# Optimization experiments

Hardware: AMD Instinct MI355X
Metric: run time of the kernel (lower is better)

Reference implementation:

```python
import jax, jax.numpy as jnp
import numpy as np

# PEPS grid configuration (matches init_kwargs)
X, Y = 4, 4            # xnodes, ynodes
D = 6                  # bond_dim
P = 2                  # features_in (physical dim)
F = 10                 # features_out (forced by result.view([10]))
CX, CY = X // 2, Y // 2  # center node carries the output leg
BATCH = 2048


def node_labels(i, j):
    # bond labels after the physical index is contracted away; axis order: up, left, down, right, out
    labs = []
    if i > 0: labs.append(f'v{i-1}_{j}')   # up bond (shared with row i-1)
    if j > 0: labs.append(f'h{i}_{j-1}')   # left bond (shared with col j-1)
    if i < X - 1: labs.append(f'v{i}_{j}') # down bond
    if j < Y - 1: labs.append(f'h{i}_{j}') # right bond
    if (i, j) == (CX, CY): labs.append('o')  # output leg on center node
    return labs


def node_shape(i, j):
    shp = [P]  # physical axis first (input_nodes[i][j][0] ^ peps_nodes[i][j][0])
    shp += [D] * (int(i > 0) + int(j > 0) + int(i < X - 1) + int(j < Y - 1))
    if (i, j) == (CX, CY): shp.append(F)
    return tuple(shp)


def setup_inputs() -> dict:
    key = jax.random.key(0)
    keys = jax.random.split(key, X * Y + 1)
    inp = {"x": jax.random.normal(keys[0], (BATCH, X, Y, P), dtype=jnp.float32)}
    k = 1
    for i in range(X):
        for j in range(Y):
            # simple_peps uniform init with std=0.01
            inp[f"w{i}{j}"] = jax.random.uniform(keys[k], node_shape(i, j), dtype=jnp.float32, minval=-0.01, maxval=0.01)
            k += 1
    return inp


def _td(a, alabs, b, blabs):
    """Label-tracked tensordot over all shared bond labels."""
    shared = [l for l in alabs if l in blabs]
    ai = [alabs.index(l) for l in shared]
    bi = [blabs.index(l) for l in shared]
    out = jnp.tensordot(a, b, axes=(ai, bi))
    labs = [l for l in alabs if l not in shared] + [l for l in blabs if l not in shared]
    return out, labs


def _contract_sample(xs, ws):
    # xs: [X, Y, P] one sample; ws: list-of-lists of node tensors
    # 1) contract each input vector into its PEPS node over the physical axis,
    #    then L2-normalize each contracted node (as in func())
    nodes = []
    for i in range(X):
        row = []
        for j in range(Y):
            t = jnp.tensordot(xs[i, j], ws[i][j], axes=(0, 0))
            t = t / jnp.linalg.norm(t)
            row.append(t)
        nodes.append(row)
    # 2) exact contraction of the 2D network, row-by-row boundary sweep
    cur, labs = nodes[0][0], node_labels(0, 0)
    for j in range(1, Y):
        cur, labs = _td(cur, labs, nodes[0][j], node_labels(0, j))
    for i in range(1, X):
        for j in range(Y):
            cur, labs = _td(cur, labs, nodes[i][j], node_labels(i, j))
    out = cur.reshape(F)  # result.view([10])
    return out / jnp.linalg.norm(out)


def reference(x, w00, w01, w02, w03, w10, w11, w12, w13,
              w20, w21, w22, w23, w30, w31, w32, w33):
    ws = [[w00, w01, w02, w03],
          [w10, w11, w12, w13],
          [w20, w21, w22, w23],
          [w30, w31, w32, w33]]
    return jax.vmap(lambda s: _contract_sample(s, ws))(x)  # [B, F]
```

## Files before the change

kernel.cpp:

```cpp
#include <hip/hip_runtime.h>
#include <math.h>

#define NTHREADS 256

struct PW {
    const float* w[16];
    int perp[16];
};

__global__ __launch_bounds__(NTHREADS) void gram64(PW pw, float* __restrict__ g) {
    const int n = blockIdx.x >> 2, sl = blockIdx.x & 3;
    const float* __restrict__ W = pw.w[n];
    const int m = pw.perp[n];
    float s00 = 0.f, s01 = 0.f, s11 = 0.f;
    for (int e = (sl * NTHREADS + threadIdx.x) * 4; e < m; e += NTHREADS * 16) {
        const float4 a = *reinterpret_cast<const float4*>(W + e);
        const float4 b = *reinterpret_cast<const float4*>(W + m + e);
        s00 += a.x * a.x + a.y * a.y + a.z * a.z + a.w * a.w;
        s01 += a.x * b.x + a.y * b.y + a.z * b.z + a.w * b.w;
        s11 += b.x * b.x + b.y * b.y + b.z * b.z + b.w * b.w;
    }
    for (int off = 32; off > 0; off >>= 1) {
        s00 += __shfl_down(s00, off, 64);
        s01 += __shfl_down(s01, off, 64);
        s11 += __shfl_down(s11, off, 64);
    }
    __shared__ float red[4][3];
    const int lane = threadIdx.x & 63, wv = threadIdx.x >> 6;
    if (lane == 0) { red[wv][0] = s00; red[wv][1] = s01; red[wv][2] = s11; }
    __syncthreads();
    if (threadIdx.x == 0) {
        float t0 = 0.f, t1 = 0.f, t2 = 0.f;
        for (int i = 0; i < 4; i++) { t0 += red[i][0]; t1 += red[i][1]; t2 += red[i][2]; }
        g[n * 12 + sl * 3 + 0] = t0; g[n * 12 + sl * 3 + 1] = t1; g[n * 12 + sl * 3 + 2] = t2;
    }
}

constexpr int SA = 0, SB = 1296, SC = 2592;
constexpr int SP = 3888, SQ = 4104, SX = 4320, SY = 4536, SZ = 4752;
constexpr int ARENA = 4968;

template<int TOT, int DST>
__device__ __forceinline__ void stg_id(float* __restrict__ lds, const float* __restrict__ W,
                                       float a0, float b0, float a1, float b1, int tid) {
    constexpr int QUADS = TOT / 4;
    for (int e = tid; e < 2 * QUADS; e += NTHREADS) {
        const int s = (e >= QUADS);
        const int p = e - s * QUADS;
        const float al = s ? a1 : a0, be = s ? b1 : b0;
        const float4 u0 = *reinterpret_cast<const float4*>(W + 4 * p);
        const float4 u1 = *reinterpret_cast<const float4*>(W + TOT + 4 * p);
        float4 rv;
        rv.x = al * u0.x + be * u1.x; rv.y = al * u0.y + be * u1.y;
        rv.z = al * u0.z + be * u1.z; rv.w = al * u0.w + be * u1.w;
        *reinterpret_cast<float4*>(lds + s * ARENA + DST + 4 * p) = rv;
    }
}

template<int D0, int D1, int D2, int D3, int S0, int S1, int S2, int S3, int DST>
__device__ __forceinline__ void stg_pm(float* __restrict__ lds, const float* __restrict__ W,
                                       float a0, float b0, float a1, float b1, int tid) {
    constexpr int TOT = D0 * D1 * D2 * D3;
    for (int e = tid; e < 2 * TOT; e += NTHREADS) {
        const int s = (e >= TOT);
        const int d = e - s * TOT;
        int r = d;
        const int i3 = r % D3; r /= D3;
        const int i2 = r % D2; r /= D2;
        const int i1 = r % D1;
        const int i0 = r / D1;
        const int src = i0 * S0 + i1 * S1 + i2 * S2 + i3 * S3;
        const float al = s ? a1 : a0, be = s ? b1 : b0;
        lds[s * ARENA + DST + d] = al * W[src] + be * W[TOT + src];
    }
}

template<int M, int N, int K, int TM, int TN, int AOFF, int BOFF>
__device__ __forceinline__ void mm_acc(const float* __restrict__ lds, int tid,
                                       float (&acc)[TM][TN]) {
    constexpr int WM = M / TM, WN = N / TN, PER_S = WM * WN, TOT = 2 * PER_S;
    static_assert(TOT <= NTHREADS, "tile overflow");
    static_assert(M % TM == 0 && N % TN == 0, "tile divide");
    if (tid >= TOT) return;
    const int s = (tid >= PER_S);
    const int r = tid - s * PER_S;
    const int mt = r / WN, nt = r - mt * WN;
    const float* __restrict__ Ab = lds + s * ARENA + AOFF + mt * TM;
    const float* __restrict__ Bb = lds + s * ARENA + BOFF + nt * TN;
#pragma unroll
    for (int i = 0; i < TM; i++)
#pragma unroll
        for (int j = 0; j < TN; j++) acc[i][j] = 0.f;
#pragma unroll 6
    for (int k = 0; k < K; ++k) {
        float a[TM], b[TN];
        if constexpr (TM == 4) {
            const float4 v = *reinterpret_cast<const float4*>(Ab + k * M);
            a[0] = v.x; a[1] = v.y; a[2] = v.z; a[3] = v.w;
        } else {
            const float2 v = *reinterpret_cast<const float2*>(Ab + k * M);
            a[0] = v.x; a[1] = v.y;
        }
        if constexpr (TN == 4) {
            const float4 v = *reinterpret_cast<const float4*>(Bb + k * N);
            b[0] = v.x; b[1] = v.y; b[2] = v.z; b[3] = v.w;
        } else {
            const float2 v = *reinterpret_cast<const float2*>(Bb + k * N);
            b[0] = v.x; b[1] = v.y;
        }
#pragma unroll
        for (int i = 0; i < TM; i++)
#pragma unroll
            for (int j = 0; j < TN; j++) acc[i][j] += a[i] * b[j];
    }
}

template<int M, int N, int TM, int TN,
         int NM2, int OSM1, int OSM2, int NN2, int OSN1, int OSN2, int OOFF>
__device__ __forceinline__ void mm_wr(float* __restrict__ lds, int tid,
                                      const float (&acc)[TM][TN]) {
    constexpr int WM = M / TM, WN = N / TN, PER_S = WM * WN, TOT = 2 * PER_S;
    if (tid >= TOT) return;
    const int s = (tid >= PER_S);
    const int r = tid - s * PER_S;
    const int mt = r / WN, nt = r - mt * WN;
    float* __restrict__ Ob = lds + s * ARENA + OOFF;
    constexpr bool NCONT = (TN == 4) && (OSN2 == 1) && ((NN2 >= N) || (OSN1 == NN2));
    constexpr bool MCONT = (TM == 4) && (OSM2 == 1) && ((NM2 >= M) || (OSM1 == NM2));
    if constexpr (NCONT) {
        const int nb = nt * TN;
#pragma unroll
        for (int i = 0; i < TM; i++) {
            const int m = mt * TM + i;
            int m1, m2;
            if constexpr (NM2 >= M) { m1 = 0; m2 = m; }
            else                    { m1 = m / NM2; m2 = m - m1 * NM2; }
            float4 v; v.x = acc[i][0]; v.y = acc[i][1]; v.z = acc[i][2]; v.w = acc[i][3];
            *reinterpret_cast<float4*>(Ob + m1 * OSM1 + m2 * OSM2 + nb) = v;
        }
    } else if constexpr (MCONT) {
        const int mb = mt * TM;
#pragma unroll
        for (int j = 0; j < TN; j++) {
            const int n = nt * TN + j;
            int n1, n2;
            if constexpr (NN2 >= N) { n1 = 0; n2 = n; }
            else                    { n1 = n / NN2; n2 = n - n1 * NN2; }
            float4 v; v.x = acc[0][j]; v.y = acc[1][j]; v.z = acc[2][j]; v.w = acc[3][j];
            *reinterpret_cast<float4*>(Ob + n1 * OSN1 + n2 * OSN2 + mb) = v;
        }
    } else {
#pragma unroll
        for (int i = 0; i < TM; i++) {
            const int m = mt * TM + i;
            int m1, m2;
            if constexpr (NM2 >= M) { m1 = 0; m2 = m; }
            else                    { m1 = m / NM2; m2 = m - m1 * NM2; }
#pragma unroll
            for (int j = 0; j < TN; j++) {
                const int n = nt * TN + j;
                int n1, n2;
                if constexpr (NN2 >= N) { n1 = 0; n2 = n; }
                else                    { n1 = n / NN2; n2 = n - n1 * NN2; }
                Ob[m1 * OSM1 + m2 * OSM2 + n1 * OSN1 + n2 * OSN2] = acc[i][j];
            }
        }
    }
}

template<int M, int N, int K, int TM, int TN,
         int NM2, int OSM1, int OSM2, int NN2, int OSN1, int OSN2,
         int AOFF, int BOFF, int OOFF>
__device__ __forceinline__ void mmd(float* __restrict__ lds, int tid) {
    float acc[TM][TN];
    mm_acc<M, N, K, TM, TN, AOFF, BOFF>(lds, tid, acc);
    mm_wr<M, N, TM, TN, NM2, OSM1, OSM2, NN2, OSN1, OSN2, OOFF>(lds, tid, acc);
}

__global__ __launch_bounds__(NTHREADS, 4) void peps_main(const float* __restrict__ x, PW pw,
                                                         const float* __restrict__ gram,
                                                         float* __restrict__ out) {
    __shared__ float lds[2 * ARENA];
    __shared__ float cfa[2][16], cfb[2][16];
    __shared__ float red[4][2][10];

    const int tid = threadIdx.x;
    const int s0 = blockIdx.x * 2;

    if (tid < 32) {
        const int sl = tid >> 4, n = tid & 15;
        const float a = x[(s0 + sl) * 32 + n * 2 + 0];
        const float b = x[(s0 + sl) * 32 + n * 2 + 1];
        float g0 = 0.f, g1 = 0.f, g2 = 0.f;
#pragma unroll
        for (int q = 0; q < 4; q++) {
            g0 += gram[n * 12 + q * 3 + 0];
            g1 += gram[n * 12 + q * 3 + 1];
            g2 += gram[n * 12 + q * 3 + 2];
        }
        const float inv = 1.f / sqrtf(a * a * g0 + 2.f * a * b * g1 + b * b * g2);
        cfa[sl][n] = a * inv; cfb[sl][n] = b * inv;
    }
    __syncthreads();

#define CF(WI) cfa[0][WI], cfb[0][WI], cfa[1][WI], cfb[1][WI]

    stg_pm<1, 1, 6, 6, 0, 0, 1, 6, SQ + 0>(lds, pw.w[0], CF(0), tid);
    stg_id<216, SX>(lds, pw.w[1], CF(1), tid);
    stg_id<216, SY>(lds, pw.w[4], CF(4), tid);
    stg_id<1296, SA>(lds, pw.w[5], CF(5), tid);
    __syncthreads();

    mmd<6, 36, 6, 2, 4, 6, 0, 36, 36, 0, 1, SQ + 0, SX, SP>(lds, tid);
    stg_pm<1, 6, 6, 6, 0, 1, 36, 6, SZ>(lds, pw.w[2], CF(2), tid);
    stg_id<36, SQ + 36>(lds, pw.w[3], CF(3), tid);
    __syncthreads();

    mmd<36, 36, 6, 4, 4, 6, 216, 6, 6, 1, 36, SP, SY, SB>(lds, tid);
    stg_id<216, SX>(lds, pw.w[7], CF(7), tid);
    stg_pm<6, 6, 6, 6, 216, 1, 36, 6, SC>(lds, pw.w[6], CF(6), tid);
    stg_id<36, SQ + 72>(lds, pw.w[12], CF(12), tid);
    __syncthreads();

    {
        float a3[4][4];
        mm_acc<36, 36, 36, 4, 4, SB, SA>(lds, tid, a3);
        mmd<36, 6, 6, 4, 2, 36, 0, 1, 6, 0, 36, SZ, SQ + 36, SP>(lds, tid);
        stg_pm<1, 6, 6, 6, 0, 6, 36, 1, SY>(lds, pw.w[8], CF(8), tid);
        __syncthreads();
        mm_wr<36, 36, 4, 4, 6, 216, 6, 6, 1, 36, SA>(lds, tid, a3);
    }
    __syncthreads();

    mmd<36, 36, 6, 4, 4, 6, 6, 216, 6, 36, 1, SP, SX, SB>(lds, tid);
    stg_pm<1, 6, 6, 6, 0, 6, 36, 1, SZ>(lds, pw.w[13], CF(13), tid);
    __syncthreads();

    {
        float a6[4][4];
        mm_acc<36, 36, 36, 4, 4, SC, SB>(lds, tid, a6);
        mmd<6, 36, 6, 2, 4, 6, 0, 36, 36, 0, 1, SQ + 72, SY, SP>(lds, tid);
        stg_id<36, SQ + 108>(lds, pw.w[15], CF(15), tid);
        stg_pm<1, 6, 6, 6, 0, 1, 36, 6, SX>(lds, pw.w[11], CF(11), tid);
        __syncthreads();
        mm_wr<36, 36, 4, 4, 6, 36, 6, 6, 216, 1, SB>(lds, tid, a6);
    }
    __syncthreads();

    {
        float a7[4][4];
        mm_acc<36, 36, 36, 4, 4, SA, SB>(lds, tid, a7);
        stg_pm<6, 6, 6, 6, 36, 6, 216, 1, SC>(lds, pw.w[9], CF(9), tid);
        stg_pm<1, 6, 6, 6, 0, 1, 36, 6, SY>(lds, pw.w[14], CF(14), tid);
        __syncthreads();
        mm_wr<36, 36, 4, 4, 6, 216, 36, 6, 6, 1, SA>(lds, tid, a7);
    }
    __syncthreads();

    {
        float a12[4][2];
        mm_acc<36, 6, 6, 4, 2, SX, SQ + 108>(lds, tid, a12);
        mmd<36, 36, 6, 4, 4, 6, 6, 216, 6, 36, 1, SP, SZ, SB>(lds, tid);
        __syncthreads();
        mm_wr<36, 6, 4, 2, 36, 0, 1, 6, 0, 36, SQ>(lds, tid, a12);
    }
    __syncthreads();

    {
        float a10[4][4], a13[4][4];
        mm_acc<36, 36, 36, 4, 4, SB, SC>(lds, tid, a10);
        mm_acc<36, 36, 6, 4, 4, SQ, SY>(lds, tid, a13);
        __syncthreads();
        mm_wr<36, 36, 4, 4, 6, 216, 6, 6, 36, 1, SC>(lds, tid, a10);
        mm_wr<36, 36, 4, 4, 6, 216, 1, 6, 6, 36, SB>(lds, tid, a13);
    }
    __syncthreads();

    {
        float a11[4][4];
        mm_acc<36, 36, 36, 4, 4, SA, SC>(lds, tid, a11);
        __syncthreads();
        mm_wr<36, 36, 4, 4, 6, 6, 216, 6, 36, 1, SA>(lds, tid, a11);
    }
    __syncthreads();

    {
        float a14[4][4];
        mm_acc<36, 36, 36, 4, 4, SA, SB>(lds, tid, a14);
        __syncthreads();
        mm_wr<36, 36, 4, 4, 6, 216, 36, 6, 6, 1, SA>(lds, tid, a14);
    }
    __syncthreads();

    {
        const float a0 = cfa[0][10], b0 = cfb[0][10];
        const float a1 = cfa[1][10], b1 = cfb[1][10];
        const float* __restrict__ w0 = pw.w[10];
        const float* __restrict__ w1 = w0 + 12960;
        float p0[10], p1[10];
#pragma unroll
        for (int o = 0; o < 10; o++) { p0[o] = 0.f; p1[o] = 0.f; }
        for (int f = tid; f < 324; f += NTHREADS) {
            const float4 E0 = *reinterpret_cast<const float4*>(lds + SA + 4 * f);
            const float4 E1 = *reinterpret_cast<const float4*>(lds + ARENA + SA + 4 * f);
            const float e0[4] = {E0.x, E0.y, E0.z, E0.w};
            const float e1[4] = {E1.x, E1.y, E1.z, E1.w};
#pragma unroll
            for (int u = 0; u < 4; u++) {
                const int e = 4 * f + u;
                const float* __restrict__ q0 = w0 + e * 10;
                const float* __restrict__ q1 = w1 + e * 10;
#pragma unroll
                for (int o = 0; o < 10; o++) {
                    const float v0 = q0[o], v1 = q1[o];
                    p0[o] += e0[u] * (a0 * v0 + b0 * v1);
                    p1[o] += e1[u] * (a1 * v0 + b1 * v1);
                }
            }
        }
#pragma unroll
        for (int o = 0; o < 10; o++)
            for (int off = 32; off > 0; off >>= 1) {
                p0[o] += __shfl_down(p0[o], off, 64);
                p1[o] += __shfl_down(p1[o], off, 64);
            }
        const int lane = tid & 63, wv = tid >> 6;
        if (lane == 0) {
#pragma unroll
            for (int o = 0; o < 10; o++) { red[wv][0][o] = p0[o]; red[wv][1][o] = p1[o]; }
        }
        __syncthreads();
        if (tid < 2) {
            float r[10];
            float ss = 0.f;
#pragma unroll
            for (int o = 0; o < 10; o++) {
                r[o] = red[0][tid][o] + red[1][tid][o] + red[2][tid][o] + red[3][tid][o];
                ss += r[o] * r[o];
            }
            const float inv = 1.f / sqrtf(ss);
#pragma unroll
            for (int o = 0; o < 10; o++) out[(s0 + tid) * 10 + o] = r[o] * inv;
        }
    }
#undef CF
}

extern "C" void kernel_launch(void* const* d_in, const int* in_sizes, int n_in,
                              void* d_out, int out_size, void* d_ws, size_t ws_size,
                              hipStream_t stream) {
    PW pw;
    for (int k = 0; k < 16; k++) {
        pw.w[k] = (const float*)d_in[1 + k];
        pw.perp[k] = in_sizes[1 + k] / 2;
    }
    float* gram = (float*)d_ws;
    gram64<<<64, NTHREADS, 0, stream>>>(pw, gram);

    const float* x = (const float*)d_in[0];
    const int B = out_size / 10;
    peps_main<<<B / 2, NTHREADS, 0, stream>>>(x, pw, gram, (float*)d_out);
}
```

Measured before the change: 134.3 us.

## Read weight operands directly from global in matmuls and reorder contraction schedule

Adds matmul variants that fold the physical-index contraction (alpha*W0 + beta*W1) into the operand load straight from global memory, so identity-layout node tensors are no longer staged into LDS first. The contraction order is also reorganised to match: the LDS arena is re-laid out, stg_id is removed, and the number of barrier-separated phases changes. The aim is to cut LDS staging traffic and some barriers. In exchange, every thread tile now re-reads weights from global/L2 inside the inner loop, which may cost more than the staging it replaces.

```diff
diff --git a/kernel.cpp b/kernel.cpp
--- a/kernel.cpp
+++ b/kernel.cpp
@@ -36,26 +36,9 @@
     }
 }
 
-constexpr int SA = 0, SB = 1296, SC = 2592;
-constexpr int SP = 3888, SQ = 4104, SX = 4320, SY = 4536, SZ = 4752;
-constexpr int ARENA = 4968;
-
-template<int TOT, int DST>
-__device__ __forceinline__ void stg_id(float* __restrict__ lds, const float* __restrict__ W,
-                                       float a0, float b0, float a1, float b1, int tid) {
-    constexpr int QUADS = TOT / 4;
-    for (int e = tid; e < 2 * QUADS; e += NTHREADS) {
-        const int s = (e >= QUADS);
-        const int p = e - s * QUADS;
-        const float al = s ? a1 : a0, be = s ? b1 : b0;
-        const float4 u0 = *reinterpret_cast<const float4*>(W + 4 * p);
-        const float4 u1 = *reinterpret_cast<const float4*>(W + TOT + 4 * p);
-        float4 rv;
-        rv.x = al * u0.x + be * u1.x; rv.y = al * u0.y + be * u1.y;
-        rv.z = al * u0.z + be * u1.z; rv.w = al * u0.w + be * u1.w;
-        *reinterpret_cast<float4*>(lds + s * ARENA + DST + 4 * p) = rv;
-    }
-}
+constexpr int SA = 0, SB = 1296, SC = 2592, SP = 3888;
+constexpr int W0A = 4104, W2A = 4140, W20A = 4356, W31A = 4572, W3A = 4788;
+constexpr int ARENA = 5004;
 
 template<int D0, int D1, int D2, int D3, int S0, int S1, int S2, int S3, int DST>
 __device__ __forceinline__ void stg_pm(float* __restrict__ lds, const float* __restrict__ W,
@@ -80,7 +63,6 @@
                                        float (&acc)[TM][TN]) {
     constexpr int WM = M / TM, WN = N / TN, PER_S = WM * WN, TOT = 2 * PER_S;
     static_assert(TOT <= NTHREADS, "tile overflow");
-    static_assert(M % TM == 0 && N % TN == 0, "tile divide");
     if (tid >= TOT) return;
     const int s = (tid >= PER_S);
     const int r = tid - s * PER_S;
@@ -100,6 +82,96 @@
         } else {
             const float2 v = *reinterpret_cast<const float2*>(Ab + k * M);
             a[0] = v.x; a[1] = v.y;
+        }
+        if constexpr (TN == 4) {
+            const float4 v = *reinterpret_cast<const float4*>(Bb + k * N);
+            b[0] = v.x; b[1] = v.y; b[2] = v.z; b[3] = v.w;
+        } else {
+            const float2 v = *reinterpret_cast<const float2*>(Bb + k * N);
+            b[0] = v.x; b[1] = v.y;
+        }
+#pragma unroll
+        for (int i = 0; i < TM; i++)
+#pragma unroll
+            for (int j = 0; j < TN; j++) acc[i][j] += a[i] * b[j];
+    }
+}
+
+template<int M, int N, int K, int TM, int TN, int AOFF, int PL>
+__device__ __forceinline__ void mm_accGB(const float* __restrict__ lds,
+                                         const float* __restrict__ W,
+                                         float a0, float b0, float a1, float b1,
+                                         int tid, float (&acc)[TM][TN]) {
+    constexpr int WM = M / TM, WN = N / TN, PER_S = WM * WN, TOT = 2 * PER_S;
+    static_assert(TOT <= NTHREADS, "tile overflow");
+    if (tid >= TOT) return;
+    const int s = (tid >= PER_S);
+    const int r = tid - s * PER_S;
+    const int mt = r / WN, nt = r - mt * WN;
+    const float al = s ? a1 : a0, be = s ? b1 : b0;
+    const float* __restrict__ Ab = lds + s * ARENA + AOFF + mt * TM;
+    const float* __restrict__ Bb = W + nt * TN;
+#pragma unroll
+    for (int i = 0; i < TM; i++)
+#pragma unroll
+        for (int j = 0; j < TN; j++) acc[i][j] = 0.f;
+#pragma unroll 6
+    for (int k = 0; k < K; ++k) {
+        float a[TM], b[TN];
+        if constexpr (TM == 4) {
+            const float4 v = *reinterpret_cast<const float4*>(Ab + k * M);
+            a[0] = v.x; a[1] = v.y; a[2] = v.z; a[3] = v.w;
+        } else {
+            const float2 v = *reinterpret_cast<const float2*>(Ab + k * M);
+            a[0] = v.x; a[1] = v.y;
+        }
+        if constexpr (TN == 4) {
+            const float4 u0 = *reinterpret_cast<const float4*>(Bb + k * N);
+            const float4 u1 = *reinterpret_cast<const float4*>(Bb + PL + k * N);
+            b[0] = al * u0.x + be * u1.x; b[1] = al * u0.y + be * u1.y;
+            b[2] = al * u0.z + be * u1.z; b[3] = al * u0.w + be * u1.w;
+        } else {
+            const float2 u0 = *reinterpret_cast<const float2*>(Bb + k * N);
+            const float2 u1 = *reinterpret_cast<const float2*>(Bb + PL + k * N);
+            b[0] = al * u0.x + be * u1.x; b[1] = al * u0.y + be * u1.y;
+        }
+#pragma unroll
+        for (int i = 0; i < TM; i++)
+#pragma unroll
+            for (int j = 0; j < TN; j++) acc[i][j] += a[i] * b[j];
+    }
+}
+
+template<int M, int N, int K, int TM, int TN, int BOFF, int PL>
+__device__ __forceinline__ void mm_accGA(const float* __restrict__ lds,
+                                         const float* __restrict__ W,
+                                         float a0, float b0, float a1, float b1,
+                                         int tid, float (&acc)[TM][TN]) {
+    constexpr int WM = M / TM, WN = N / TN, PER_S = WM * WN, TOT = 2 * PER_S;
+    static_assert(TOT <= NTHREADS, "tile overflow");
+    if (tid >= TOT) return;
+    const int s = (tid >= PER_S);
+    const int r = tid - s * PER_S;
+    const int mt = r / WN, nt = r - mt * WN;
+    const float al = s ? a1 : a0, be = s ? b1 : b0;
+    const float* __restrict__ Ab = W + mt * TM;
+    const float* __restrict__ Bb = lds + s * ARENA + BOFF + nt * TN;
+#pragma unroll
+    for (int i = 0; i < TM; i++)
+#pragma unroll
+        for (int j = 0; j < TN; j++) acc[i][j] = 0.f;
+#pragma unroll 6
+    for (int k = 0; k < K; ++k) {
+        float a[TM], b[TN];
+        if constexpr (TM == 4) {
+            const float4 u0 = *reinterpret_cast<const float4*>(Ab + k * M);
+            const float4 u1 = *reinterpret_cast<const float4*>(Ab + PL + k * M);
+            a[0] = al * u0.x + be * u1.x; a[1] = al * u0.y + be * u1.y;
+            a[2] = al * u0.z + be * u1.z; a[3] = al * u0.w + be * u1.w;
+        } else {
+            const float2 u0 = *reinterpret_cast<const float2*>(Ab + k * M);
+            const float2 u1 = *reinterpret_cast<const float2*>(Ab + PL + k * M);
+            a[0] = al * u0.x + be * u1.x; a[1] = al * u0.y + be * u1.y;
         }
         if constexpr (TN == 4) {
             const float4 v = *reinterpret_cast<const float4*>(Bb + k * N);
@@ -177,6 +249,26 @@
     mm_wr<M, N, TM, TN, NM2, OSM1, OSM2, NN2, OSN1, OSN2, OOFF>(lds, tid, acc);
 }
 
+template<int M, int N, int K, int TM, int TN,
+         int NM2, int OSM1, int OSM2, int NN2, int OSN1, int OSN2,
+         int AOFF, int PL, int OOFF>
+__device__ __forceinline__ void mmdGB(float* __restrict__ lds, const float* __restrict__ W,
+                                      float a0, float b0, float a1, float b1, int tid) {
+    float acc[TM][TN];
+    mm_accGB<M, N, K, TM, TN, AOFF, PL>(lds, W, a0, b0, a1, b1, tid, acc);
+    mm_wr<M, N, TM, TN, NM2, OSM1, OSM2, NN2, OSN1, OSN2, OOFF>(lds, tid, acc);
+}
+
+template<int M, int N, int K, int TM, int TN,
+         int NM2, int OSM1, int OSM2, int NN2, int OSN1, int OSN2,
+         int BOFF, int PL, int OOFF>
+__device__ __forceinline__ void mmdGA(float* __restrict__ lds, const float* __restrict__ W,
+                                      float a0, float b0, float a1, float b1, int tid) {
+    float acc[TM][TN];
+    mm_accGA<M, N, K, TM, TN, BOFF, PL>(lds, W, a0, b0, a1, b1, tid, acc);
+    mm_wr<M, N, TM, TN, NM2, OSM1, OSM2, NN2, OSN1, OSN2, OOFF>(lds, tid, acc);
+}
+
 __global__ __launch_bounds__(NTHREADS, 4) void peps_main(const float* __restrict__ x, PW pw,
                                                          const float* __restrict__ gram,
                                                          float* __restrict__ out) {
@@ -205,91 +297,65 @@
 
 #define CF(WI) cfa[0][WI], cfb[0][WI], cfa[1][WI], cfb[1][WI]
 
-    stg_pm<1, 1, 6, 6, 0, 0, 1, 6, SQ + 0>(lds, pw.w[0], CF(0), tid);
-    stg_id<216, SX>(lds, pw.w[1], CF(1), tid);
-    stg_id<216, SY>(lds, pw.w[4], CF(4), tid);
-    stg_id<1296, SA>(lds, pw.w[5], CF(5), tid);
-    __syncthreads();
-
-    mmd<6, 36, 6, 2, 4, 6, 0, 36, 36, 0, 1, SQ + 0, SX, SP>(lds, tid);
-    stg_pm<1, 6, 6, 6, 0, 1, 36, 6, SZ>(lds, pw.w[2], CF(2), tid);
-    stg_id<36, SQ + 36>(lds, pw.w[3], CF(3), tid);
-    __syncthreads();
-
-    mmd<36, 36, 6, 4, 4, 6, 216, 6, 6, 1, 36, SP, SY, SB>(lds, tid);
-    stg_id<216, SX>(lds, pw.w[7], CF(7), tid);
     stg_pm<6, 6, 6, 6, 216, 1, 36, 6, SC>(lds, pw.w[6], CF(6), tid);
-    stg_id<36, SQ + 72>(lds, pw.w[12], CF(12), tid);
-    __syncthreads();
-
-    {
-        float a3[4][4];
-        mm_acc<36, 36, 36, 4, 4, SB, SA>(lds, tid, a3);
-        mmd<36, 6, 6, 4, 2, 36, 0, 1, 6, 0, 36, SZ, SQ + 36, SP>(lds, tid);
-        stg_pm<1, 6, 6, 6, 0, 6, 36, 1, SY>(lds, pw.w[8], CF(8), tid);
-        __syncthreads();
-        mm_wr<36, 36, 4, 4, 6, 216, 6, 6, 1, 36, SA>(lds, tid, a3);
-    }
-    __syncthreads();
-
-    mmd<36, 36, 6, 4, 4, 6, 6, 216, 6, 36, 1, SP, SX, SB>(lds, tid);
-    stg_pm<1, 6, 6, 6, 0, 6, 36, 1, SZ>(lds, pw.w[13], CF(13), tid);
+    stg_pm<1, 1, 6, 6, 0, 0, 1, 6, W0A>(lds, pw.w[0], CF(0), tid);
+    stg_pm<1, 6, 6, 6, 0, 1, 36, 6, W2A>(lds, pw.w[2], CF(2), tid);
+    stg_pm<1, 6, 6, 6, 0, 6, 36, 1, W20A>(lds, pw.w[8], CF(8), tid);
+    stg_pm<1, 6, 6, 6, 0, 6, 36, 1, W31A>(lds, pw.w[13], CF(13), tid);
+    stg_pm<1, 6, 6, 6, 0, 1, 36, 6, W3A>(lds, pw.w[14], CF(14), tid);
+    __syncthreads();
+
+    mmdGB<6, 36, 6, 2, 4, 6, 0, 36, 36, 0, 1, W0A, 216, SP>(lds, pw.w[1], CF(1), tid);
+    __syncthreads();
+
+    mmdGB<36, 36, 6, 4, 4, 6, 216, 6, 6, 1, 36, SP, 216, SA>(lds, pw.w[4], CF(4), tid);
+    __syncthreads();
+
+    mmdGB<36, 36, 36, 4, 4, 6, 216, 6, 6, 1, 36, SA, 1296, SB>(lds, pw.w[5], CF(5), tid);
+    mmdGB<36, 6, 6, 4, 2, 36, 0, 1, 6, 0, 36, W2A, 36, SP>(lds, pw.w[3], CF(3), tid);
+    __syncthreads();
+
+    mmdGB<36, 36, 6, 4, 4, 6, 6, 216, 6, 36, 1, SP, 216, SA>(lds, pw.w[7], CF(7), tid);
     __syncthreads();
 
     {
         float a6[4][4];
-        mm_acc<36, 36, 36, 4, 4, SC, SB>(lds, tid, a6);
-        mmd<6, 36, 6, 2, 4, 6, 0, 36, 36, 0, 1, SQ + 72, SY, SP>(lds, tid);
-        stg_id<36, SQ + 108>(lds, pw.w[15], CF(15), tid);
-        stg_pm<1, 6, 6, 6, 0, 1, 36, 6, SX>(lds, pw.w[11], CF(11), tid);
+        mm_acc<36, 36, 36, 4, 4, SC, SA>(lds, tid, a6);
         __syncthreads();
-        mm_wr<36, 36, 4, 4, 6, 36, 6, 6, 216, 1, SB>(lds, tid, a6);
+        mm_wr<36, 36, 4, 4, 6, 36, 6, 6, 216, 1, SA>(lds, tid, a6);
     }
     __syncthreads();
 
     {
         float a7[4][4];
-        mm_acc<36, 36, 36, 4, 4, SA, SB>(lds, tid, a7);
+        mm_acc<36, 36, 36, 4, 4, SB, SA>(lds, tid, a7);
         stg_pm<6, 6, 6, 6, 36, 6, 216, 1, SC>(lds, pw.w[9], CF(9), tid);
-        stg_pm<1, 6, 6, 6, 0, 1, 36, 6, SY>(lds, pw.w[14], CF(14), tid);
+        mmdGA<6, 36, 6, 2, 4, 6, 0, 36, 36, 0, 1, W20A, 36, SP>(lds, pw.w[12], CF(12), tid);
         __syncthreads();
-        mm_wr<36, 36, 4, 4, 6, 216, 36, 6, 6, 1, SA>(lds, tid, a7);
-    }
+        mm_wr<36, 36, 4, 4, 6, 216, 36, 6, 6, 1, SB>(lds, tid, a7);
+    }
+    __syncthreads();
+
+    mmd<36, 36, 6, 4, 4, 6, 6, 216, 6, 36, 1, SP, W31A, SA>(lds, tid);
+    stg_pm<1, 6, 6, 6, 0, 1, 36, 6, W2A>(lds, pw.w[11], CF(11), tid);
     __syncthreads();
 
     {
-        float a12[4][2];
-        mm_acc<36, 6, 6, 4, 2, SX, SQ + 108>(lds, tid, a12);
-        mmd<36, 36, 6, 4, 4, 6, 6, 216, 6, 36, 1, SP, SZ, SB>(lds, tid);
+        float a10[4][4];
+        mm_acc<36, 36, 36, 4, 4, SA, SC>(lds, tid, a10);
         __syncthreads();
-        mm_wr<36, 6, 4, 2, 36, 0, 1, 6, 0, 36, SQ>(lds, tid, a12);
-    }
-    __syncthreads();
-
-    {
-        float a10[4][4], a13[4][4];
-        mm_acc<36, 36, 36, 4, 4, SB, SC>(lds, tid, a10);
-        mm_acc<36, 36, 6, 4, 4, SQ, SY>(lds, tid, a13);
-        __syncthreads();
-        mm_wr<36, 36, 4, 4, 6, 216, 6, 6, 36, 1, SC>(lds, tid, a10);
-        mm_wr<36, 36, 4, 4, 6, 216, 1, 6, 6, 36, SB>(lds, tid, a13);
-    }
-    __syncthreads();
-
-    {
-        float a11[4][4];
-        mm_acc<36, 36, 36, 4, 4, SA, SC>(lds, tid, a11);
-        __syncthreads();
-        mm_wr<36, 36, 4, 4, 6, 6, 216, 6, 36, 1, SA>(lds, tid, a11);
-    }
-    __syncthreads();
-
-    {
-        float a14[4][4];
-        mm_acc<36, 36, 36, 4, 4, SA, SB>(lds, tid, a14);
-        __syncthreads();
-        mm_wr<36, 36, 4, 4, 6, 216, 36, 6, 6, 1, SA>(lds, tid, a14);
-    }
+        mm_wr<36, 36, 4, 4, 6, 216, 6, 6, 36, 1, SA>(lds, tid, a10);
+    }
+    __syncthreads();
+
+    mmd<36, 36, 36, 4, 4, 6, 6, 216, 6, 36, 1, SB, SA, SC>(lds, tid);
+    mmdGB<36, 6, 6, 4, 2, 36, 0, 1, 6, 0, 36, W2A, 36, SP>(lds, pw.w[15], CF(15), tid);
+    __syncthreads();
+
+    mmd<36, 36, 6, 4, 4, 6, 216, 1, 6, 6, 36, SP, W3A, SB>(lds, tid);
+    __syncthreads();
+
+    mmd<36, 36, 36, 4, 4, 6, 216, 36, 6, 6, 1, SC, SB, SA>(lds, tid);
     __syncthreads();
 
     {
```

After: 140.6 us. 4.7% more time.
